# Kernel optimization log

Measured on AMD Instinct MI355X. Metric: run time of the kernel, lower is better.

## Reference

```python
import jax, jax.numpy as jnp
import numpy as np

B, L, IN, D = 256, 256, 256, 128


def setup_inputs() -> dict:
    key = jax.random.key(0)
    ks = jax.random.split(key, 12)

    def U(k, shape, fan):
        s = 1.0 / np.sqrt(fan)
        return jax.random.uniform(k, shape, jnp.float32, -s, s)

    x = jax.random.normal(ks[0], (B, L, IN), jnp.float32)
    # cor[b,t] indexes the hidden-state history; must lie in [0, t]
    cor = jnp.minimum(jax.random.randint(ks[1], (B, L), 0, L),
                      jnp.arange(L)[None, :]).astype(jnp.int32)
    w_r = U(ks[2], (D, IN), IN); b_r = U(ks[3], (D,), IN); u_r = U(ks[4], (D, D), D)
    w_z = U(ks[5], (D, IN), IN); b_z = U(ks[6], (D,), IN); u_z = U(ks[7], (D, D), D)
    w_h = U(ks[8], (D, IN), IN); b_h = U(ks[9], (D,), IN); u_h = U(ks[10], (D, D), D)
    k1k2 = U(ks[11], (2, IN), IN)
    return dict(x=x, cor=cor, w_r=w_r, b_r=b_r, u_r=u_r,
                w_z=w_z, b_z=b_z, u_z=u_z, w_h=w_h, b_h=b_h, u_h=u_h,
                k1k2=k1k2)


def reference(x, cor, w_r, b_r, u_r, w_z, b_z, u_z, w_h, b_h, u_h, k1k2):
    Bs, Ls, _ = x.shape
    Dd = w_r.shape[0]
    Hh = Dd // 2
    # input projections for all timesteps at once (torch does them per-step)
    Xr = jnp.einsum('bli,di->bld', x, w_r) + b_r
    Xz = jnp.einsum('bli,di->bld', x, w_z) + b_z
    Xh = jnp.einsum('bli,di->bld', x, w_h) + b_h
    a = jax.nn.softmax(jnp.einsum('bli,ki->blk', x, k1k2), axis=-1)[..., 0:1]  # [B,L,1]
    bidx = jnp.arange(Bs)
    buf0 = jnp.zeros((Ls + 1, Bs, Hh), x.dtype)  # second halves of hid_states[j]
    h0 = jnp.zeros((Bs, Dd), x.dtype)

    def step(carry, inp):
        buf, h_prev = carry
        t, xr, xz, xh, at, ct = inp
        # cor==0 aliases to hid_states[-1] == h_{t-1} (stored at buf[t])
        i_eff = jnp.where(ct == 0, t, ct)
        m2 = buf[i_eff, bidx]                       # h_y[:, D/2:]  [B, D/2]
        m_t = jnp.concatenate([at * h_prev[:, :Hh], (1.0 - at) * m2], axis=1)
        r = jax.nn.sigmoid(xr + m_t @ u_r.T)
        z = jax.nn.sigmoid(xz + m_t @ u_z.T)
        hh = jnp.tanh(xh + r * (m_t @ u_h.T))
        h = (1.0 - z) * m_t + z * hh
        buf = jax.lax.dynamic_update_index_in_dim(buf, h[:, Hh:], t + 1, 0)
        return (buf, h), h

    ts = jnp.arange(Ls)
    xs = (ts, jnp.moveaxis(Xr, 1, 0), jnp.moveaxis(Xz, 1, 0),
          jnp.moveaxis(Xh, 1, 0), jnp.moveaxis(a, 1, 0), cor.T)
    _, hs = jax.lax.scan(step, (buf0, h0), xs)    # hs: [L, B, D]
    return jnp.transpose(hs, (1, 0, 2))           # [B, L, D]
```

## Files before the change

kernel.cpp:

```cpp
#include <hip/hip_runtime.h>

typedef float f32x4 __attribute__((ext_vector_type(4)));
typedef _Float16 f16x8 __attribute__((ext_vector_type(8)));
typedef _Float16 f16x4 __attribute__((ext_vector_type(4)));
typedef _Float16 f16x2 __attribute__((ext_vector_type(2)));

#define NB 256
#define NL 256
#define NIN 256
#define ND 128
#define NH 64
#define CH 16
#define AXP 280

#define BAR_LDS()                                                     \
  do {                                                                \
    asm volatile("s_waitcnt lgkmcnt(0)\n\ts_barrier" ::: "memory");   \
    __builtin_amdgcn_sched_barrier(0);                                \
  } while (0)

__global__ void kwpack_kernel(const float* __restrict__ w_r,
                              const float* __restrict__ w_z,
                              const float* __restrict__ w_h,
                              _Float16* __restrict__ wpk) {
  const int lane = threadIdx.x;
  const int nt = blockIdx.x;
  const int kc = blockIdx.y;
  const float* wg = (nt < 8) ? w_r : (nt < 16) ? w_z : w_h;
  const int col = (nt & 7) * 16 + (lane & 15);
  const int k0 = kc * 32 + (lane >> 4) * 8;
  const float4* p = (const float4*)(wg + (size_t)col * NIN + k0);
  float4 v0 = p[0], v1 = p[1];
  f16x8 f;
  f[0] = (_Float16)v0.x; f[1] = (_Float16)v0.y;
  f[2] = (_Float16)v0.z; f[3] = (_Float16)v0.w;
  f[4] = (_Float16)v1.x; f[5] = (_Float16)v1.y;
  f[6] = (_Float16)v1.z; f[7] = (_Float16)v1.w;
  *(f16x8*)&wpk[(((size_t)nt * 8 + kc) * 64 + lane) * 8] = f;
}

__global__ __launch_bounds__(1024) void kscan_kernel(
    const float* __restrict__ u_r, const float* __restrict__ u_z,
    const float* __restrict__ u_h, const float* __restrict__ b_r,
    const float* __restrict__ b_z, const float* __restrict__ b_h,
    const int* __restrict__ cor, const float* __restrict__ x,
    const _Float16* __restrict__ wpk, const float* __restrict__ k1k2,
    float* __restrict__ out) {
  const int b = blockIdx.x;
  const int tid = threadIdx.x;
  const int lane = tid & 63;
  const int w = tid >> 6;
  const bool scanw = (w < 8);
  const int pw = w - 8;
  const int quad = lane >> 4;
  const int l16 = lane & 15;
  const int q8 = quad * 8;

  __shared__ __align__(16) _Float16 hist[(NL + 1) * NH];
  __shared__ __align__(16) _Float16 Xl[2 * 3 * CH * ND];
  __shared__ __align__(16) _Float16 Axt[16 * AXP];
  __shared__ __align__(16) _Float16 hprev16[2][NH];
  __shared__ float sA[NL];
  __shared__ int sIeff[NL];
  __shared__ float k12f[NIN];

  const size_t rowb = (size_t)b * NL;

  if (tid < NH) { hprev16[0][tid] = (_Float16)0.f; hist[tid] = (_Float16)0.f; }
  if (tid < NL) {
    const int c = cor[rowb + tid];
    sIeff[tid] = (c == 0) ? tid : c;
  }
  if (tid < NIN) k12f[tid] = k1k2[tid] - k1k2[NIN + tid];

  const int prow0 = 2 * pw;
  float4 xrA0, xrB0;
  f32x4 accP = (f32x4){0.f, 0.f, 0.f, 0.f};

  auto LOADX = [&](int t0) {
    const float4* pa = (const float4*)(x + (rowb + t0 + prow0) * NIN + lane * 4);
    const float4* pb = (const float4*)(x + (rowb + t0 + prow0 + 1) * NIN + lane * 4);
    xrA0 = pa[0];
    xrB0 = pb[0];
  };
  auto STAGEX = [&](int t0) {
    f16x4 ha, hb;
    ha[0] = (_Float16)xrA0.x; ha[1] = (_Float16)xrA0.y;
    ha[2] = (_Float16)xrA0.z; ha[3] = (_Float16)xrA0.w;
    hb[0] = (_Float16)xrB0.x; hb[1] = (_Float16)xrB0.y;
    hb[2] = (_Float16)xrB0.z; hb[3] = (_Float16)xrB0.w;
    *(f16x4*)&Axt[prow0 * AXP + lane * 4] = ha;
    *(f16x4*)&Axt[(prow0 + 1) * AXP + lane * 4] = hb;
    const float4 kk = *(const float4*)&k12f[lane * 4];
    float pa = xrA0.x * kk.x + xrA0.y * kk.y + xrA0.z * kk.z + xrA0.w * kk.w;
    float pb = xrB0.x * kk.x + xrB0.y * kk.y + xrB0.z * kk.z + xrB0.w * kk.w;
#pragma unroll
    for (int s = 1; s < 64; s <<= 1) {
      pa += __shfl_xor(pa, s);
      pb += __shfl_xor(pb, s);
    }
    if (lane == 0) {
      sA[t0 + prow0] = 1.f / (1.f + __expf(-pa));
      sA[t0 + prow0 + 1] = 1.f / (1.f + __expf(-pb));
    }
  };
  auto GEMM_HALF = [&](int i, int half, int buf) {
    const int nt = pw * 3 + i;
    f16x8 bfr[4];
#pragma unroll
    for (int kk = 0; kk < 4; ++kk)
      bfr[kk] = *(const f16x8*)
          &wpk[(((size_t)nt * 8 + half * 4 + kk) * 64 + lane) * 8];
    if (half == 0) accP = (f32x4){0.f, 0.f, 0.f, 0.f};
#pragma unroll
    for (int kk = 0; kk < 4; ++kk) {
      f16x8 af = *(const f16x8*)&Axt[l16 * AXP + (half * 4 + kk) * 32 + q8];
      accP = __builtin_amdgcn_mfma_f32_16x16x32_f16(af, bfr[kk], accP, 0, 0, 0);
    }
    if (half == 1) {
      const int g = nt >> 3;
      const int dblk = nt & 7;
      _Float16* xd = &Xl[((buf * 3 + g) * CH + quad * 4) * ND + dblk * 16 + l16];
#pragma unroll
      for (int r = 0; r < 4; ++r) xd[r * ND] = (_Float16)accP[r];
    }
  };

  if (!scanw) LOADX(0);
  __syncthreads();
  if (!scanw) STAGEX(0);
  __syncthreads();
  if (!scanw) {
    GEMM_HALF(0, 0, 0); GEMM_HALF(0, 1, 0);
    GEMM_HALF(1, 0, 0); GEMM_HALF(1, 1, 0);
    GEMM_HALF(2, 0, 0); GEMM_HALF(2, 1, 0);
  }
  __syncthreads();

  if (scanw) {
    f16x8 bf[3][4];
#pragma unroll
    for (int g = 0; g < 3; ++g) {
      const float* ug = (g == 0) ? u_r : (g == 1) ? u_z : u_h;
      const float* base = ug + (size_t)(16 * w + l16) * ND;
#pragma unroll
      for (int kk = 0; kk < 4; ++kk) {
        const float4* p = (const float4*)(base + kk * 32 + q8);
        float4 v0 = p[0], v1 = p[1];
        f16x8 f;
        f[0] = (_Float16)v0.x; f[1] = (_Float16)v0.y;
        f[2] = (_Float16)v0.z; f[3] = (_Float16)v0.w;
        f[4] = (_Float16)v1.x; f[5] = (_Float16)v1.y;
        f[6] = (_Float16)v1.z; f[7] = (_Float16)v1.w;
        bf[g][kk] = f;
      }
    }

    const bool owner = (quad == 0);
    const int d = 16 * w + l16;
    float bbv[3] = {0.f, 0.f, 0.f};
    if (owner) { bbv[0] = b_r[d]; bbv[1] = b_z[d]; bbv[2] = b_h[d]; }

    const f32x4 kZ = (f32x4){0.f, 0.f, 0.f, 0.f};
    float a_c = sA[0];
    int ieff_c = sIeff[0];
    bool pf_c = true;
    float hp = 0.f;
    f32x4 accL[3], accH[3];
#pragma unroll
    for (int g = 0; g < 3; ++g) { accL[g] = kZ; accH[g] = kZ; }

    for (int t = 0; t < NL; ++t) {
      const int par = t & 1;
      const float a = a_c;
      const float oma = 1.f - a;
      const int ieff = ieff_c;
      const int cur = (t >> 4) & 1;
      const int tin = t & 15;

      if (!pf_c) {
        f16x8 g2 = *(const f16x8*)&hist[ieff * NH + q8];
        f16x8 g3 = *(const f16x8*)&hist[ieff * NH + 32 + q8];
#pragma unroll
        for (int g = 0; g < 3; ++g) {
          accH[g] = __builtin_amdgcn_mfma_f32_16x16x32_f16(g2, bf[g][2], kZ, 0, 0, 0);
          accH[g] = __builtin_amdgcn_mfma_f32_16x16x32_f16(g3, bf[g][3], accH[g], 0, 0, 0);
        }
      }

      f16x8 h0 = *(const f16x8*)&hprev16[par][q8];
      f16x8 h1 = *(const f16x8*)&hprev16[par][32 + q8];
#pragma unroll
      for (int g = 0; g < 3; ++g) {
        accL[g] = __builtin_amdgcn_mfma_f32_16x16x32_f16(h0, bf[g][0], kZ, 0, 0, 0);
        accL[g] = __builtin_amdgcn_mfma_f32_16x16x32_f16(h1, bf[g][1], accL[g], 0, 0, 0);
      }

      float xv[3], md = 0.f;
      if (owner) {
#pragma unroll
        for (int g = 0; g < 3; ++g)
          xv[g] = (float)Xl[((cur * 3 + g) * CH + tin) * ND + d];
        if (w < 4) {
          md = a * hp;
        } else if (ieff == t) {
          md = oma * hp;
        } else {
          md = oma * (float)hist[ieff * NH + (d - NH)];
        }
      }

      const int tn = (t < NL - 1) ? t + 1 : t;
      float a_n = sA[tn];
      int ieff_n = sIeff[tn];
      bool pf_n = (ieff_n <= t);

      if (owner) {
        float mr = a * accL[0][0] + oma * accH[0][0];
        float mz = a * accL[1][0] + oma * accH[1][0];
        float mh = a * accL[2][0] + oma * accH[2][0];
        float er = __expf(-(xv[0] + bbv[0] + mr));
        float rr = __builtin_amdgcn_rcpf(1.f + er);
        float ez = __expf(-(xv[1] + bbv[1] + mz));
        float zz = __builtin_amdgcn_rcpf(1.f + ez);
        float e2 = __expf(2.f * (xv[2] + bbv[2] + rr * mh));
        float hh = (e2 - 1.f) * __builtin_amdgcn_rcpf(e2 + 1.f);
        float h = md + zz * (hh - md);
        hp = h;
        out[(rowb + t) * ND + d] = h;
        if (d < NH) hprev16[par ^ 1][d] = (_Float16)h;
        else        hist[(t + 1) * NH + (d - NH)] = (_Float16)h;
      }

      if (pf_n) {
        f16x8 g2 = *(const f16x8*)&hist[ieff_n * NH + q8];
        f16x8 g3 = *(const f16x8*)&hist[ieff_n * NH + 32 + q8];
#pragma unroll
        for (int g = 0; g < 3; ++g) {
          accH[g] = __builtin_amdgcn_mfma_f32_16x16x32_f16(g2, bf[g][2], kZ, 0, 0, 0);
          accH[g] = __builtin_amdgcn_mfma_f32_16x16x32_f16(g3, bf[g][3], accH[g], 0, 0, 0);
        }
      }

      BAR_LDS();
      a_c = a_n; ieff_c = ieff_n; pf_c = pf_n;
    }
  } else {
    for (int t = 0; t < NL; ++t) {
      const int tin = t & 15;
      const int t0n = (t & ~15) + 16;
      if (t0n < NL) {
        const int bufn = (t0n >> 4) & 1;
        if (tin == 0)      LOADX(t0n);
        else if (tin == 2) STAGEX(t0n);
        else if (tin >= 3 && tin <= 8) {
          const int i = (tin - 3) >> 1;
          const int half = (tin - 3) & 1;
          GEMM_HALF(i, half, bufn);
        }
      }
      BAR_LDS();
    }
  }
}

extern "C" void kernel_launch(void* const* d_in, const int* in_sizes, int n_in,
                              void* d_out, int out_size, void* d_ws, size_t ws_size,
                              hipStream_t stream) {
  (void)in_sizes; (void)n_in; (void)out_size; (void)ws_size;
  const float* x    = (const float*)d_in[0];
  const int*   cor  = (const int*)d_in[1];
  const float* w_r  = (const float*)d_in[2];
  const float* b_r  = (const float*)d_in[3];
  const float* u_r  = (const float*)d_in[4];
  const float* w_z  = (const float*)d_in[5];
  const float* b_z  = (const float*)d_in[6];
  const float* u_z  = (const float*)d_in[7];
  const float* w_h  = (const float*)d_in[8];
  const float* b_h  = (const float*)d_in[9];
  const float* u_h  = (const float*)d_in[10];
  const float* k1k2 = (const float*)d_in[11];

  _Float16* wpk = (_Float16*)d_ws;

  kwpack_kernel<<<dim3(24, 8), dim3(64), 0, stream>>>(w_r, w_z, w_h, wpk);
  kscan_kernel<<<dim3(NB), dim3(1024), 0, stream>>>(u_r, u_z, u_h, b_r, b_z,
                                                    b_h, cor, x, wpk, k1k2,
                                                    (float*)d_out);
}
```

Before: 262.2 us.

## Batch history-half MFMA across 16 timesteps using all MFMA output rows

Rather than issuing a separate history-half MFMA for each timestep, the recurrent loop now computes, every 16 steps, the history contribution for all 16 upcoming timesteps in one MFMA batch. Each of the 16 A-rows gathers the history row for one timestep, clamped to a row already available. Only timesteps whose history index is too recent fall back to a per-step MFMA. The owning lane quad rotates every 4 steps so it can read the matching batched accumulator element, and md is now read from fp16 shared memory instead of the fp32 register. This cuts per-step MFMA and LDS work on the serial critical path, at the cost of the late-path branch and an fp16 rounding of md.

```diff
diff --git a/kernel.cpp b/kernel.cpp
--- a/kernel.cpp
+++ b/kernel.cpp
@@ -156,94 +156,99 @@
       }
     }
 
-    const bool owner = (quad == 0);
     const int d = 16 * w + l16;
-    float bbv[3] = {0.f, 0.f, 0.f};
-    if (owner) { bbv[0] = b_r[d]; bbv[1] = b_z[d]; bbv[2] = b_h[d]; }
+    float bbv[3];
+    bbv[0] = b_r[d]; bbv[1] = b_z[d]; bbv[2] = b_h[d];
 
     const f32x4 kZ = (f32x4){0.f, 0.f, 0.f, 0.f};
     float a_c = sA[0];
     int ieff_c = sIeff[0];
-    bool pf_c = true;
-    float hp = 0.f;
-    f32x4 accL[3], accH[3];
-#pragma unroll
-    for (int g = 0; g < 3; ++g) { accL[g] = kZ; accH[g] = kZ; }
-
-    for (int t = 0; t < NL; ++t) {
-      const int par = t & 1;
-      const float a = a_c;
-      const float oma = 1.f - a;
-      const int ieff = ieff_c;
-      const int cur = (t >> 4) & 1;
-      const int tin = t & 15;
-
-      if (!pf_c) {
-        f16x8 g2 = *(const f16x8*)&hist[ieff * NH + q8];
-        f16x8 g3 = *(const f16x8*)&hist[ieff * NH + 32 + q8];
+    f32x4 accHB[3];
+
+    for (int tb = 0; tb < NL; tb += 4) {
+      const int cur = (tb >> 4) & 1;
+      const int t0 = tb & ~15;
+      const int tinb = tb & 15;
+
+      if (tinb == 0) {
+        int ie = sIeff[t0 + l16];
+        int rv = (ie > t0) ? t0 : ie;
+        const _Float16* hrow = &hist[rv * NH];
+        f16x8 a0 = *(const f16x8*)&hrow[q8];
+        f16x8 a1 = *(const f16x8*)&hrow[32 + q8];
 #pragma unroll
         for (int g = 0; g < 3; ++g) {
-          accH[g] = __builtin_amdgcn_mfma_f32_16x16x32_f16(g2, bf[g][2], kZ, 0, 0, 0);
-          accH[g] = __builtin_amdgcn_mfma_f32_16x16x32_f16(g3, bf[g][3], accH[g], 0, 0, 0);
-        }
-      }
-
-      f16x8 h0 = *(const f16x8*)&hprev16[par][q8];
-      f16x8 h1 = *(const f16x8*)&hprev16[par][32 + q8];
-#pragma unroll
-      for (int g = 0; g < 3; ++g) {
-        accL[g] = __builtin_amdgcn_mfma_f32_16x16x32_f16(h0, bf[g][0], kZ, 0, 0, 0);
-        accL[g] = __builtin_amdgcn_mfma_f32_16x16x32_f16(h1, bf[g][1], accL[g], 0, 0, 0);
-      }
-
-      float xv[3], md = 0.f;
-      if (owner) {
-#pragma unroll
-        for (int g = 0; g < 3; ++g)
-          xv[g] = (float)Xl[((cur * 3 + g) * CH + tin) * ND + d];
-        if (w < 4) {
-          md = a * hp;
-        } else if (ieff == t) {
-          md = oma * hp;
-        } else {
-          md = oma * (float)hist[ieff * NH + (d - NH)];
-        }
-      }
-
-      const int tn = (t < NL - 1) ? t + 1 : t;
-      float a_n = sA[tn];
-      int ieff_n = sIeff[tn];
-      bool pf_n = (ieff_n <= t);
-
-      if (owner) {
-        float mr = a * accL[0][0] + oma * accH[0][0];
-        float mz = a * accL[1][0] + oma * accH[1][0];
-        float mh = a * accL[2][0] + oma * accH[2][0];
-        float er = __expf(-(xv[0] + bbv[0] + mr));
-        float rr = __builtin_amdgcn_rcpf(1.f + er);
-        float ez = __expf(-(xv[1] + bbv[1] + mz));
-        float zz = __builtin_amdgcn_rcpf(1.f + ez);
-        float e2 = __expf(2.f * (xv[2] + bbv[2] + rr * mh));
-        float hh = (e2 - 1.f) * __builtin_amdgcn_rcpf(e2 + 1.f);
-        float h = md + zz * (hh - md);
-        hp = h;
-        out[(rowb + t) * ND + d] = h;
-        if (d < NH) hprev16[par ^ 1][d] = (_Float16)h;
-        else        hist[(t + 1) * NH + (d - NH)] = (_Float16)h;
-      }
-
-      if (pf_n) {
-        f16x8 g2 = *(const f16x8*)&hist[ieff_n * NH + q8];
-        f16x8 g3 = *(const f16x8*)&hist[ieff_n * NH + 32 + q8];
+          accHB[g] = __builtin_amdgcn_mfma_f32_16x16x32_f16(a0, bf[g][2], kZ, 0, 0, 0);
+          accHB[g] = __builtin_amdgcn_mfma_f32_16x16x32_f16(a1, bf[g][3], accHB[g], 0, 0, 0);
+        }
+      }
+
+      const int oq = tinb >> 2;
+      const bool owner = (quad == oq);
+
+#pragma unroll
+      for (int j = 0; j < 4; ++j) {
+        const int t = tb + j;
+        const int par = j & 1;
+        const int tin = tinb + j;
+        const float a = a_c;
+        const float oma = 1.f - a;
+        const int ieff = ieff_c;
+        const bool late = (ieff > t0);
+
+        f32x4 hl0, hl1, hl2;
+        if (late) {
+          f16x8 g2 = *(const f16x8*)&hist[ieff * NH + q8];
+          f16x8 g3 = *(const f16x8*)&hist[ieff * NH + 32 + q8];
+          hl0 = __builtin_amdgcn_mfma_f32_16x16x32_f16(g2, bf[0][2], kZ, 0, 0, 0);
+          hl0 = __builtin_amdgcn_mfma_f32_16x16x32_f16(g3, bf[0][3], hl0, 0, 0, 0);
+          hl1 = __builtin_amdgcn_mfma_f32_16x16x32_f16(g2, bf[1][2], kZ, 0, 0, 0);
+          hl1 = __builtin_amdgcn_mfma_f32_16x16x32_f16(g3, bf[1][3], hl1, 0, 0, 0);
+          hl2 = __builtin_amdgcn_mfma_f32_16x16x32_f16(g2, bf[2][2], kZ, 0, 0, 0);
+          hl2 = __builtin_amdgcn_mfma_f32_16x16x32_f16(g3, bf[2][3], hl2, 0, 0, 0);
+        }
+
+        f16x8 h0 = *(const f16x8*)&hprev16[par][q8];
+        f16x8 h1 = *(const f16x8*)&hprev16[par][32 + q8];
+        f32x4 accL[3];
 #pragma unroll
         for (int g = 0; g < 3; ++g) {
-          accH[g] = __builtin_amdgcn_mfma_f32_16x16x32_f16(g2, bf[g][2], kZ, 0, 0, 0);
-          accH[g] = __builtin_amdgcn_mfma_f32_16x16x32_f16(g3, bf[g][3], accH[g], 0, 0, 0);
-        }
-      }
-
-      BAR_LDS();
-      a_c = a_n; ieff_c = ieff_n; pf_c = pf_n;
+          accL[g] = __builtin_amdgcn_mfma_f32_16x16x32_f16(h0, bf[g][0], kZ, 0, 0, 0);
+          accL[g] = __builtin_amdgcn_mfma_f32_16x16x32_f16(h1, bf[g][1], accL[g], 0, 0, 0);
+        }
+
+        const int tn = (t < NL - 1) ? t + 1 : t;
+        float a_n = sA[tn];
+        int ieff_n = sIeff[tn];
+
+        if (owner) {
+          float xv0 = (float)Xl[((cur * 3 + 0) * CH + tin) * ND + d];
+          float xv1 = (float)Xl[((cur * 3 + 1) * CH + tin) * ND + d];
+          float xv2 = (float)Xl[((cur * 3 + 2) * CH + tin) * ND + d];
+          float md;
+          if (w < 4) md = a * (float)hprev16[par][d];
+          else       md = oma * (float)hist[ieff * NH + (d - NH)];
+          float H0 = late ? hl0[0] : accHB[0][j];
+          float H1 = late ? hl1[0] : accHB[1][j];
+          float H2 = late ? hl2[0] : accHB[2][j];
+          float mr = a * accL[0][0] + oma * H0;
+          float mz = a * accL[1][0] + oma * H1;
+          float mh = a * accL[2][0] + oma * H2;
+          float er = __expf(-(xv0 + bbv[0] + mr));
+          float rr = __builtin_amdgcn_rcpf(1.f + er);
+          float ez = __expf(-(xv1 + bbv[1] + mz));
+          float zz = __builtin_amdgcn_rcpf(1.f + ez);
+          float e2 = __expf(2.f * (xv2 + bbv[2] + rr * mh));
+          float hh = (e2 - 1.f) * __builtin_amdgcn_rcpf(e2 + 1.f);
+          float h = md + zz * (hh - md);
+          out[(rowb + t) * ND + d] = h;
+          if (d < NH) hprev16[par ^ 1][d] = (_Float16)h;
+          else        hist[(t + 1) * NH + (d - NH)] = (_Float16)h;
+        }
+
+        BAR_LDS();
+        a_c = a_n; ieff_c = ieff_n;
+      }
     }
   } else {
     for (int t = 0; t < NL; ++t) {
```

New measurement: 239.9 us. -8.5%, faster.
